# Optimization experiments

Measured on AMD Instinct MI355X. Metric: run time of the kernel, lower is better.

The kernel has to match this reference:

```python
import jax, jax.numpy as jnp
import numpy as np
from jax import lax

B, T, H, CTX, CONV_OUT = 32, 1536, 1024, 1024, 32


def setup_inputs() -> dict:
    key = jax.random.key(0)
    ks = jax.random.split(key, 10)
    s = 1.0 / np.sqrt(H)
    return {
        "decoder_output": jax.random.normal(ks[0], (B, 1, H), jnp.float32),
        "encoder_outputs": jax.random.normal(ks[1], (B, T, H), jnp.float32),
        "last_alignment": jax.random.uniform(ks[2], (B, T), jnp.float32),
        "W": jax.random.normal(ks[3], (CTX, H), jnp.float32) * s,
        "V": jax.random.normal(ks[4], (CTX, H), jnp.float32) * s,
        "U": jax.random.normal(ks[5], (CTX, CONV_OUT), jnp.float32) * (1.0 / np.sqrt(CONV_OUT)),
        "b": jax.random.uniform(ks[6], (CTX,), jnp.float32, -0.1, 0.1),
        "w": jax.random.normal(ks[7], (CTX,), jnp.float32) * (1.0 / np.sqrt(CTX)),
        "conv_w": jax.random.normal(ks[8], (CONV_OUT, 1, 3), jnp.float32) * 0.5,
        "conv_b": jax.random.normal(ks[9], (CONV_OUT,), jnp.float32) * 0.1,
    }


def reference(decoder_output, encoder_outputs, last_alignment, W, V, U, b, w, conv_w, conv_b):
    # location feature: Conv1d(1 -> conv_out, k=3, pad=1) over previous alignment
    conv = lax.conv_general_dilated(
        last_alignment[:, None, :], conv_w,
        window_strides=(1,), padding=[(1, 1)],
        dimension_numbers=("NCW", "OIW", "NCW"),
    ) + conv_b[None, :, None]                      # (B, conv_out, T)
    loc = jnp.transpose(conv, (0, 2, 1))           # (B, T, conv_out)

    # additive (Bahdanau) energies: (B,1,ctx) + (B,T,ctx) + (B,T,ctx) + (ctx,)
    e = jnp.tanh(
        jnp.einsum("bqh,ch->bqc", decoder_output, W)
        + jnp.einsum("bth,ch->btc", encoder_outputs, V)
        + jnp.einsum("btk,ck->btc", loc, U)
        + b
    )                                              # (B, T, ctx)
    scores = jnp.einsum("btc,c->bt", e, w)         # (B, T)
    alignment = jax.nn.softmax(scores, axis=-1)    # (B, T)
    context = jnp.einsum("bt,bth->bh", alignment, encoder_outputs)  # (B, H)
    return context, alignment
```

## Files before the change

kernel.cpp:

```cpp
#include <hip/hip_runtime.h>
#include <hip/hip_bf16.h>
#include <hip/hip_fp16.h>


constexpr int kB = 32, kT = 1536, kH = 1024, kC = 1024, kCO = 32;
constexpr int kM = kB * kT;
constexpr int kKp = 1088;

typedef _Float16 f16;
typedef _Float16 f16x8 __attribute__((ext_vector_type(8)));
typedef float f32x4 __attribute__((ext_vector_type(4)));

constexpr size_t W2_A     = 0;
constexpr size_t W2_B     = W2_A + (size_t)kM * kKp * 2;
constexpr size_t W2_ADD   = W2_B + (size_t)kC * kKp * 2;
constexpr size_t W2_SCORE = W2_ADD + (size_t)kB * kC * 4;
constexpr size_t W2_CTXP  = W2_SCORE + (size_t)8 * kM * 4;

__device__ __forceinline__ void gload16(const void* g, void* l) {
    __builtin_amdgcn_global_load_lds(
        (const __attribute__((address_space(1))) void*)g,
        (__attribute__((address_space(3))) void*)l, 16, 0, 0);
}

__global__ void k_cvt(const float* __restrict__ enc, f16* __restrict__ Af) {
    int gid = blockIdx.x * 256 + threadIdx.x;
    int row = gid >> 7, c8 = gid & 127;
    const float* src = enc + (size_t)row * kH + c8 * 8;
    float4 e0 = *(const float4*)src;
    float4 e1 = *(const float4*)(src + 4);
    union { f16 h[8]; int4 q; } u;
    u.h[0] = (f16)e0.x; u.h[1] = (f16)e0.y; u.h[2] = (f16)e0.z; u.h[3] = (f16)e0.w;
    u.h[4] = (f16)e1.x; u.h[5] = (f16)e1.y; u.h[6] = (f16)e1.z; u.h[7] = (f16)e1.w;
    *(int4*)(Af + (size_t)row * kKp + c8 * 8) = u.q;
}

__global__ void k_loc(const float* __restrict__ la, const float* __restrict__ cw,
                      const float* __restrict__ cb, f16* __restrict__ Af) {
    int m = blockIdx.x * 256 + threadIdx.x;
    int b = m / kT, t = m - b * kT;
    float x0 = (t > 0)      ? la[(size_t)b * kT + t - 1] : 0.f;
    float x1 = la[(size_t)b * kT + t];
    float x2 = (t < kT - 1) ? la[(size_t)b * kT + t + 1] : 0.f;
    union { f16 h[32]; int4 q[4]; } u;
#pragma unroll
    for (int k = 0; k < 32; ++k)
        u.h[k] = (f16)(cw[k * 3] * x0 + cw[k * 3 + 1] * x1 + cw[k * 3 + 2] * x2 + cb[k]);
    int4* dst = (int4*)(Af + (size_t)m * kKp + kH);
    dst[0] = u.q[0]; dst[1] = u.q[1]; dst[2] = u.q[2]; dst[3] = u.q[3];
    int4 z = {0, 0, 0, 0};
    dst[4] = z; dst[5] = z; dst[6] = z; dst[7] = z;
}

__global__ void k_prep_b2(const float* __restrict__ V, const float* __restrict__ U,
                          f16* __restrict__ Bf) {
    int c = blockIdx.x;
    for (int k = threadIdx.x; k < kKp; k += 256) {
        float v = (k < kH) ? V[(size_t)c * kH + k]
                : (k < kH + kCO) ? U[(size_t)c * kCO + (k - kH)] : 0.f;
        Bf[(size_t)c * kKp + k] = (f16)v;
    }
}

__global__ void k_prep_add(const float* __restrict__ dec, const float* __restrict__ W,
                           const float* __restrict__ bias, float* __restrict__ add) {
    __shared__ float dl[kH];
    int bb = blockIdx.x >> 2;
    int cc = (blockIdx.x & 3) * 256 + threadIdx.x;
    *(float4*)&dl[threadIdx.x * 4] = *(const float4*)&dec[(size_t)bb * kH + threadIdx.x * 4];
    __syncthreads();
    float acc = bias[cc];
    const float* wr = W + (size_t)cc * kH;
    for (int h = 0; h < kH; h += 4) {
        float4 wv = *(const float4*)&wr[h];
        acc += wv.x * dl[h] + wv.y * dl[h + 1] + wv.z * dl[h + 2] + wv.w * dl[h + 3];
    }
    add[(size_t)bb * kC + cc] = acc;
}

__launch_bounds__(256, 4)
__global__ void k_main(const f16* __restrict__ Ag, const f16* __restrict__ Bg,
                       const float* __restrict__ add, const float* __restrict__ wvec,
                       float* __restrict__ spart) {
    __shared__ __align__(16) char smem[34816];
    float* add_l = (float*)(smem + 32768);
    float* w_l   = (float*)(smem + 33280);
    float (*sred)[64][2] = (float (*)[64][2])(smem + 33792);

    const int tid = threadIdx.x, lane = tid & 63, wave = tid >> 6;
    const int wm = wave >> 1, wn = wave & 1;
    const int raw = blockIdx.x;
    const int lin = (raw & 7) * 384 + (raw >> 3);
    const int mt = lin >> 3, nt = lin & 7;
    const int m0 = mt * 128, n0 = nt * 128;
    const int bb = m0 / kT;

    if (tid < 128) {
        add_l[tid] = add[(size_t)bb * kC + n0 + tid];
        w_l[tid]   = wvec[n0 + tid];
    }

    f32x4 acc[4][4];
#pragma unroll
    for (int i = 0; i < 4; ++i)
#pragma unroll
        for (int j = 0; j < 4; ++j) acc[i][j] = (f32x4){0.f, 0.f, 0.f, 0.f};

    const int rG = lane >> 3;
    const int gc = (lane & 7) ^ (rG & 7);
    const f16* aS[4]; const f16* bS[4];
#pragma unroll
    for (int j = 0; j < 4; ++j) {
        aS[j] = Ag + (size_t)(m0 + wave * 32 + j * 8 + rG) * kKp + gc * 8;
        bS[j] = Bg + (size_t)(n0 + wave * 32 + j * 8 + rG) * kKp + gc * 8;
    }
    const unsigned aDst = wave * 4096u;
    const unsigned bDst = 16384u + wave * 4096u;
    const int g = lane >> 4, rl = lane & 15;

    for (int t = 0; t < 17; ++t) {
#pragma unroll
        for (int j = 0; j < 4; ++j) gload16(aS[j] + t * 64, smem + aDst + j * 1024);
#pragma unroll
        for (int j = 0; j < 4; ++j) gload16(bS[j] + t * 64, smem + bDst + j * 1024);
        __syncthreads();
#pragma unroll
        for (int kk = 0; kk < 2; ++kk) {
            f16x8 bfv[4], af[4];
#pragma unroll
            for (int ni = 0; ni < 4; ++ni)
                bfv[ni] = *(const f16x8*)(smem + 16384 + (wn * 64 + ni * 16 + rl) * 128
                                          + (((kk * 4 + g) ^ (rl & 7)) << 4));
#pragma unroll
            for (int mi = 0; mi < 4; ++mi)
                af[mi] = *(const f16x8*)(smem + (wm * 64 + mi * 16 + rl) * 128
                                         + (((kk * 4 + g) ^ (rl & 7)) << 4));
            __builtin_amdgcn_s_setprio(1);
#pragma unroll
            for (int mi = 0; mi < 4; ++mi)
#pragma unroll
                for (int ni = 0; ni < 4; ++ni)
                    acc[mi][ni] = __builtin_amdgcn_mfma_f32_16x16x32_f16(af[mi], bfv[ni], acc[mi][ni], 0, 0, 0);
            __builtin_amdgcn_s_setprio(0);
        }
        __syncthreads();
    }

#pragma unroll
    for (int mi = 0; mi < 4; ++mi) {
#pragma unroll
        for (int i = 0; i < 4; ++i) {
            float p = 0.f;
#pragma unroll
            for (int ni = 0; ni < 4; ++ni) {
                int cl = wn * 64 + ni * 16 + rl;
                float e = tanhf(acc[mi][ni][i] + add_l[cl]);
                p += e * w_l[cl];
            }
            p += __shfl_xor(p, 1);
            p += __shfl_xor(p, 2);
            p += __shfl_xor(p, 4);
            p += __shfl_xor(p, 8);
            if (rl == 0) sred[wm][mi * 16 + g * 4 + i][wn] = p;
        }
    }
    __syncthreads();
    if (tid < 128) {
        int r = tid & 63, w2 = tid >> 6;
        float s = sred[w2][r][0] + sred[w2][r][1];
        spart[(size_t)nt * kM + m0 + tid] = s;
    }
}

__global__ void k_softmax(const float* __restrict__ spart, float* __restrict__ out_align) {
    __shared__ float red[256];
    int b = blockIdx.x, tid = threadIdx.x;
    float v[6];
    float mx = -1e30f;
#pragma unroll
    for (int i = 0; i < 6; ++i) {
        size_t idx = (size_t)b * kT + tid + i * 256;
        float s = 0.f;
#pragma unroll
        for (int p = 0; p < 8; ++p) s += spart[(size_t)p * kM + idx];
        v[i] = s; mx = fmaxf(mx, s);
    }
    red[tid] = mx; __syncthreads();
    for (int o = 128; o > 0; o >>= 1) { if (tid < o) red[tid] = fmaxf(red[tid], red[tid + o]); __syncthreads(); }
    mx = red[0]; __syncthreads();
    float sum = 0.f;
#pragma unroll
    for (int i = 0; i < 6; ++i) { v[i] = expf(v[i] - mx); sum += v[i]; }
    red[tid] = sum; __syncthreads();
    for (int o = 128; o > 0; o >>= 1) { if (tid < o) red[tid] += red[tid + o]; __syncthreads(); }
    float inv = 1.f / red[0];
#pragma unroll
    for (int i = 0; i < 6; ++i)
        out_align[(size_t)b * kT + tid + i * 256] = v[i] * inv;
}

__global__ void k_ctx_part(const f16* __restrict__ Af, const float* __restrict__ align,
                           float* __restrict__ cpart) {
    __shared__ float al[192];
    int ci = blockIdx.x, b = blockIdx.y, tid = threadIdx.x;
    if (tid < 192) al[tid] = align[(size_t)b * kT + ci * 192 + tid];
    __syncthreads();
    float4 acc = {0.f, 0.f, 0.f, 0.f};
    const f16* ep = Af + ((size_t)b * kT + (size_t)ci * 192) * kKp + tid * 4;
    for (int t = 0; t < 192; ++t) {
        float a = al[t];
        f16 e0 = ep[(size_t)t * kKp + 0], e1 = ep[(size_t)t * kKp + 1];
        f16 e2 = ep[(size_t)t * kKp + 2], e3 = ep[(size_t)t * kKp + 3];
        acc.x += a * (float)e0; acc.y += a * (float)e1;
        acc.z += a * (float)e2; acc.w += a * (float)e3;
    }
    *(float4*)&cpart[((size_t)ci * kB + b) * kH + tid * 4] = acc;
}

__global__ void k_ctx_red(const float* __restrict__ cpart, float* __restrict__ out_ctx) {
    int idx = blockIdx.x * 256 + threadIdx.x;
    float s = 0.f;
#pragma unroll
    for (int ci = 0; ci < 8; ++ci) s += cpart[(size_t)ci * kB * kH + idx];
    out_ctx[idx] = s;
}

extern "C" void kernel_launch(void* const* d_in, const int* in_sizes, int n_in,
                              void* d_out, int out_size, void* d_ws, size_t ws_size,
                              hipStream_t stream) {
    const float* dec  = (const float*)d_in[0];
    const float* enc  = (const float*)d_in[1];
    const float* la   = (const float*)d_in[2];
    const float* W    = (const float*)d_in[3];
    const float* V    = (const float*)d_in[4];
    const float* U    = (const float*)d_in[5];
    const float* bias = (const float*)d_in[6];
    const float* wv   = (const float*)d_in[7];
    const float* cw   = (const float*)d_in[8];
    const float* cb   = (const float*)d_in[9];

    char* ws = (char*)d_ws;
    f16* Af      = (f16*)(ws + W2_A);
    f16* Bf      = (f16*)(ws + W2_B);
    float* add   = (float*)(ws + W2_ADD);
    float* spart = (float*)(ws + W2_SCORE);
    float* cpart = (float*)(ws + W2_CTXP);

    float* out_ctx   = (float*)d_out;
    float* out_align = (float*)d_out + kB * kH;

    hipLaunchKernelGGL(k_prep_b2,  dim3(kC),             dim3(256), 0, stream, V, U, Bf);
    hipLaunchKernelGGL(k_loc,      dim3(kM / 256),       dim3(256), 0, stream, la, cw, cb, Af);
    hipLaunchKernelGGL(k_cvt,      dim3(kM * kH / 8 / 256), dim3(256), 0, stream, enc, Af);
    hipLaunchKernelGGL(k_prep_add, dim3(kB * 4),         dim3(256), 0, stream, dec, W, bias, add);
    hipLaunchKernelGGL(k_main,     dim3((kM / 128) * 8), dim3(256), 0, stream, Af, Bf, add, wv, spart);
    hipLaunchKernelGGL(k_softmax,  dim3(kB),             dim3(256), 0, stream, spart, out_align);
    hipLaunchKernelGGL(k_ctx_part, dim3(8, kB),          dim3(256), 0, stream, Af, out_align, cpart);
    hipLaunchKernelGGL(k_ctx_red,  dim3(kB * kH / 256),  dim3(256), 0, stream, cpart, out_ctx);
}
```

Measured before the change: 239.6 us.

## Fuse encoder fp32-to-f16 conversion into GEMM A-tile loading, drop staging buffer

Removes the separate pass that converted the whole encoder tensor to a padded f16 matrix. The GEMM kernel now loads fp32 encoder rows directly, converts them to f16 in registers and writes them swizzled into LDS; the location-conv features come from a small padded buffer in a final K step. The context reduction reads fp32 encoder data with vector loads, and the V/U weight prep is vectorised. This avoids a large extra write and read of a full-size intermediate. In exchange, each A tile is re-read in fp32 (twice the bytes) by every N-tile block, and synchronous register-staged loads replace the asynchronous global-to-LDS copies.

Result: slower. 325.2 us (+35.7%).

```diff
diff --git a/kernel.cpp b/kernel.cpp
--- a/kernel.cpp
+++ b/kernel.cpp
@@ -11,11 +11,10 @@
 typedef _Float16 f16x8 __attribute__((ext_vector_type(8)));
 typedef float f32x4 __attribute__((ext_vector_type(4)));
 
-constexpr size_t W2_A     = 0;
-constexpr size_t W2_B     = W2_A + (size_t)kM * kKp * 2;
-constexpr size_t W2_ADD   = W2_B + (size_t)kC * kKp * 2;
-constexpr size_t W2_SCORE = W2_ADD + (size_t)kB * kC * 4;
-constexpr size_t W2_CTXP  = W2_SCORE + (size_t)8 * kM * 4;
+constexpr size_t WS_B    = 0;
+constexpr size_t WS_LOC  = WS_B + (size_t)kC * kKp * 2;
+constexpr size_t WS_ADD  = WS_LOC + (size_t)kM * 64 * 2;
+constexpr size_t WS_SCR  = WS_ADD + (size_t)kB * kC * 4;
 
 __device__ __forceinline__ void gload16(const void* g, void* l) {
     __builtin_amdgcn_global_load_lds(
@@ -23,20 +22,29 @@
         (__attribute__((address_space(3))) void*)l, 16, 0, 0);
 }
 
-__global__ void k_cvt(const float* __restrict__ enc, f16* __restrict__ Af) {
-    int gid = blockIdx.x * 256 + threadIdx.x;
-    int row = gid >> 7, c8 = gid & 127;
-    const float* src = enc + (size_t)row * kH + c8 * 8;
-    float4 e0 = *(const float4*)src;
-    float4 e1 = *(const float4*)(src + 4);
+__global__ void k_prep_b2(const float* __restrict__ V, const float* __restrict__ U,
+                          f16* __restrict__ Bf) {
+    int c = blockIdx.x, k8 = threadIdx.x;
+    if (k8 >= 136) return;
     union { f16 h[8]; int4 q; } u;
-    u.h[0] = (f16)e0.x; u.h[1] = (f16)e0.y; u.h[2] = (f16)e0.z; u.h[3] = (f16)e0.w;
-    u.h[4] = (f16)e1.x; u.h[5] = (f16)e1.y; u.h[6] = (f16)e1.z; u.h[7] = (f16)e1.w;
-    *(int4*)(Af + (size_t)row * kKp + c8 * 8) = u.q;
+    if (k8 < 128) {
+        const float* src = V + (size_t)c * kH + k8 * 8;
+        float4 a = *(const float4*)src, b = *(const float4*)(src + 4);
+        u.h[0] = (f16)a.x; u.h[1] = (f16)a.y; u.h[2] = (f16)a.z; u.h[3] = (f16)a.w;
+        u.h[4] = (f16)b.x; u.h[5] = (f16)b.y; u.h[6] = (f16)b.z; u.h[7] = (f16)b.w;
+    } else if (k8 < 132) {
+        const float* src = U + (size_t)c * kCO + (k8 - 128) * 8;
+        float4 a = *(const float4*)src, b = *(const float4*)(src + 4);
+        u.h[0] = (f16)a.x; u.h[1] = (f16)a.y; u.h[2] = (f16)a.z; u.h[3] = (f16)a.w;
+        u.h[4] = (f16)b.x; u.h[5] = (f16)b.y; u.h[6] = (f16)b.z; u.h[7] = (f16)b.w;
+    } else {
+        u.q = (int4){0, 0, 0, 0};
+    }
+    *(int4*)(Bf + (size_t)c * kKp + k8 * 8) = u.q;
 }
 
 __global__ void k_loc(const float* __restrict__ la, const float* __restrict__ cw,
-                      const float* __restrict__ cb, f16* __restrict__ Af) {
+                      const float* __restrict__ cb, f16* __restrict__ locPad) {
     int m = blockIdx.x * 256 + threadIdx.x;
     int b = m / kT, t = m - b * kT;
     float x0 = (t > 0)      ? la[(size_t)b * kT + t - 1] : 0.f;
@@ -46,20 +54,10 @@
 #pragma unroll
     for (int k = 0; k < 32; ++k)
         u.h[k] = (f16)(cw[k * 3] * x0 + cw[k * 3 + 1] * x1 + cw[k * 3 + 2] * x2 + cb[k]);
-    int4* dst = (int4*)(Af + (size_t)m * kKp + kH);
+    int4* dst = (int4*)(locPad + (size_t)m * 64);
     dst[0] = u.q[0]; dst[1] = u.q[1]; dst[2] = u.q[2]; dst[3] = u.q[3];
     int4 z = {0, 0, 0, 0};
     dst[4] = z; dst[5] = z; dst[6] = z; dst[7] = z;
-}
-
-__global__ void k_prep_b2(const float* __restrict__ V, const float* __restrict__ U,
-                          f16* __restrict__ Bf) {
-    int c = blockIdx.x;
-    for (int k = threadIdx.x; k < kKp; k += 256) {
-        float v = (k < kH) ? V[(size_t)c * kH + k]
-                : (k < kH + kCO) ? U[(size_t)c * kCO + (k - kH)] : 0.f;
-        Bf[(size_t)c * kKp + k] = (f16)v;
-    }
 }
 
 __global__ void k_prep_add(const float* __restrict__ dec, const float* __restrict__ W,
@@ -79,9 +77,9 @@
 }
 
 __launch_bounds__(256, 4)
-__global__ void k_main(const f16* __restrict__ Ag, const f16* __restrict__ Bg,
-                       const float* __restrict__ add, const float* __restrict__ wvec,
-                       float* __restrict__ spart) {
+__global__ void k_main(const float* __restrict__ enc, const f16* __restrict__ Bg,
+                       const f16* __restrict__ locPad, const float* __restrict__ add,
+                       const float* __restrict__ wvec, float* __restrict__ spart) {
     __shared__ __align__(16) char smem[34816];
     float* add_l = (float*)(smem + 32768);
     float* w_l   = (float*)(smem + 33280);
@@ -106,23 +104,77 @@
 #pragma unroll
         for (int j = 0; j < 4; ++j) acc[i][j] = (f32x4){0.f, 0.f, 0.f, 0.f};
 
+    const int ar = tid >> 1, ah = tid & 1;
+    const float* aSrc = enc + (size_t)(m0 + ar) * kH + ah * 32;
+    char* aw = smem + ar * 128;
+    const int axm = ar & 7;
+
     const int rG = lane >> 3;
-    const int gc = (lane & 7) ^ (rG & 7);
-    const f16* aS[4]; const f16* bS[4];
+    const int gc = (lane & 7) ^ rG;
+    const f16* bS[4];
+    const f16* aT[4];
 #pragma unroll
     for (int j = 0; j < 4; ++j) {
-        aS[j] = Ag + (size_t)(m0 + wave * 32 + j * 8 + rG) * kKp + gc * 8;
-        bS[j] = Bg + (size_t)(n0 + wave * 32 + j * 8 + rG) * kKp + gc * 8;
+        int row = wave * 32 + j * 8 + rG;
+        bS[j] = Bg + (size_t)(n0 + row) * kKp + gc * 8;
+        aT[j] = locPad + (size_t)(m0 + row) * 64 + gc * 8;
     }
     const unsigned aDst = wave * 4096u;
     const unsigned bDst = 16384u + wave * 4096u;
     const int g = lane >> 4, rl = lane & 15;
 
-    for (int t = 0; t < 17; ++t) {
-#pragma unroll
-        for (int j = 0; j < 4; ++j) gload16(aS[j] + t * 64, smem + aDst + j * 1024);
+    for (int t = 0; t < 16; ++t) {
+        const float* ap = aSrc + t * 64;
+        float4 f0 = *(const float4*)(ap);
+        float4 f1 = *(const float4*)(ap + 4);
+        float4 f2 = *(const float4*)(ap + 8);
+        float4 f3 = *(const float4*)(ap + 12);
+        float4 f4 = *(const float4*)(ap + 16);
+        float4 f5 = *(const float4*)(ap + 20);
+        float4 f6 = *(const float4*)(ap + 24);
+        float4 f7 = *(const float4*)(ap + 28);
 #pragma unroll
         for (int j = 0; j < 4; ++j) gload16(bS[j] + t * 64, smem + bDst + j * 1024);
+        union { f16 h[32]; int4 q[4]; } pk;
+        pk.h[0]  = (f16)f0.x; pk.h[1]  = (f16)f0.y; pk.h[2]  = (f16)f0.z; pk.h[3]  = (f16)f0.w;
+        pk.h[4]  = (f16)f1.x; pk.h[5]  = (f16)f1.y; pk.h[6]  = (f16)f1.z; pk.h[7]  = (f16)f1.w;
+        pk.h[8]  = (f16)f2.x; pk.h[9]  = (f16)f2.y; pk.h[10] = (f16)f2.z; pk.h[11] = (f16)f2.w;
+        pk.h[12] = (f16)f3.x; pk.h[13] = (f16)f3.y; pk.h[14] = (f16)f3.z; pk.h[15] = (f16)f3.w;
+        pk.h[16] = (f16)f4.x; pk.h[17] = (f16)f4.y; pk.h[18] = (f16)f4.z; pk.h[19] = (f16)f4.w;
+        pk.h[20] = (f16)f5.x; pk.h[21] = (f16)f5.y; pk.h[22] = (f16)f5.z; pk.h[23] = (f16)f5.w;
+        pk.h[24] = (f16)f6.x; pk.h[25] = (f16)f6.y; pk.h[26] = (f16)f6.z; pk.h[27] = (f16)f6.w;
+        pk.h[28] = (f16)f7.x; pk.h[29] = (f16)f7.y; pk.h[30] = (f16)f7.z; pk.h[31] = (f16)f7.w;
+#pragma unroll
+        for (int j = 0; j < 4; ++j)
+            *(int4*)(aw + (((ah * 4 + j) ^ axm) * 16)) = pk.q[j];
+        __syncthreads();
+#pragma unroll
+        for (int kk = 0; kk < 2; ++kk) {
+            f16x8 bfv[4], af[4];
+#pragma unroll
+            for (int ni = 0; ni < 4; ++ni)
+                bfv[ni] = *(const f16x8*)(smem + 16384 + (wn * 64 + ni * 16 + rl) * 128
+                                          + (((kk * 4 + g) ^ (rl & 7)) << 4));
+#pragma unroll
+            for (int mi = 0; mi < 4; ++mi)
+                af[mi] = *(const f16x8*)(smem + (wm * 64 + mi * 16 + rl) * 128
+                                         + (((kk * 4 + g) ^ (rl & 7)) << 4));
+            __builtin_amdgcn_s_setprio(1);
+#pragma unroll
+            for (int mi = 0; mi < 4; ++mi)
+#pragma unroll
+                for (int ni = 0; ni < 4; ++ni)
+                    acc[mi][ni] = __builtin_amdgcn_mfma_f32_16x16x32_f16(af[mi], bfv[ni], acc[mi][ni], 0, 0, 0);
+            __builtin_amdgcn_s_setprio(0);
+        }
+        __syncthreads();
+    }
+
+    {
+#pragma unroll
+        for (int j = 0; j < 4; ++j) gload16(aT[j], smem + aDst + j * 1024);
+#pragma unroll
+        for (int j = 0; j < 4; ++j) gload16(bS[j] + 1024, smem + bDst + j * 1024);
         __syncthreads();
 #pragma unroll
         for (int kk = 0; kk < 2; ++kk) {
@@ -199,20 +251,18 @@
         out_align[(size_t)b * kT + tid + i * 256] = v[i] * inv;
 }
 
-__global__ void k_ctx_part(const f16* __restrict__ Af, const float* __restrict__ align,
+__global__ void k_ctx_part(const float* __restrict__ enc, const float* __restrict__ align,
                            float* __restrict__ cpart) {
     __shared__ float al[192];
     int ci = blockIdx.x, b = blockIdx.y, tid = threadIdx.x;
     if (tid < 192) al[tid] = align[(size_t)b * kT + ci * 192 + tid];
     __syncthreads();
     float4 acc = {0.f, 0.f, 0.f, 0.f};
-    const f16* ep = Af + ((size_t)b * kT + (size_t)ci * 192) * kKp + tid * 4;
+    const float* ep = enc + ((size_t)b * kT + (size_t)ci * 192) * kH + tid * 4;
     for (int t = 0; t < 192; ++t) {
         float a = al[t];
-        f16 e0 = ep[(size_t)t * kKp + 0], e1 = ep[(size_t)t * kKp + 1];
-        f16 e2 = ep[(size_t)t * kKp + 2], e3 = ep[(size_t)t * kKp + 3];
-        acc.x += a * (float)e0; acc.y += a * (float)e1;
-        acc.z += a * (float)e2; acc.w += a * (float)e3;
+        float4 e = *(const float4*)(ep + (size_t)t * kH);
+        acc.x += a * e.x; acc.y += a * e.y; acc.z += a * e.z; acc.w += a * e.w;
     }
     *(float4*)&cpart[((size_t)ci * kB + b) * kH + tid * 4] = acc;
 }
@@ -240,21 +290,20 @@
     const float* cb   = (const float*)d_in[9];
 
     char* ws = (char*)d_ws;
-    f16* Af      = (f16*)(ws + W2_A);
-    f16* Bf      = (f16*)(ws + W2_B);
-    float* add   = (float*)(ws + W2_ADD);
-    float* spart = (float*)(ws + W2_SCORE);
-    float* cpart = (float*)(ws + W2_CTXP);
+    f16* Bf      = (f16*)(ws + WS_B);
+    f16* locPad  = (f16*)(ws + WS_LOC);
+    float* add   = (float*)(ws + WS_ADD);
+    float* spart = (float*)(ws + WS_SCR);
+    float* cpart = (float*)(ws + WS_SCR);
 
     float* out_ctx   = (float*)d_out;
     float* out_align = (float*)d_out + kB * kH;
 
     hipLaunchKernelGGL(k_prep_b2,  dim3(kC),             dim3(256), 0, stream, V, U, Bf);
-    hipLaunchKernelGGL(k_loc,      dim3(kM / 256),       dim3(256), 0, stream, la, cw, cb, Af);
-    hipLaunchKernelGGL(k_cvt,      dim3(kM * kH / 8 / 256), dim3(256), 0, stream, enc, Af);
+    hipLaunchKernelGGL(k_loc,      dim3(kM / 256),       dim3(256), 0, stream, la, cw, cb, locPad);
     hipLaunchKernelGGL(k_prep_add, dim3(kB * 4),         dim3(256), 0, stream, dec, W, bias, add);
-    hipLaunchKernelGGL(k_main,     dim3((kM / 128) * 8), dim3(256), 0, stream, Af, Bf, add, wv, spart);
+    hipLaunchKernelGGL(k_main,     dim3((kM / 128) * 8), dim3(256), 0, stream, enc, Bf, locPad, add, wv, spart);
     hipLaunchKernelGGL(k_softmax,  dim3(kB),             dim3(256), 0, stream, spart, out_align);
-    hipLaunchKernelGGL(k_ctx_part, dim3(8, kB),          dim3(256), 0, stream, Af, out_align, cpart);
+    hipLaunchKernelGGL(k_ctx_part, dim3(8, kB),          dim3(256), 0, stream, enc, out_align, cpart);
     hipLaunchKernelGGL(k_ctx_red,  dim3(kB * kH / 256),  dim3(256), 0, stream, cpart, out_ctx);
 }
```
